# Kernel optimization log

Hardware: AMD Instinct MI355X
Metric: run time of the kernel (lower is better)

Reference implementation:

```python
import jax, jax.numpy as jnp
import numpy as np

NUM_BLOCKS = 100  # original samples at most 100 blocks; ids are in [0, NUM_BLOCKS)
EPS = 1e-8       # F.cosine_similarity default eps (clamps norms from below)


def setup_inputs() -> dict:
    key = jax.random.key(0)
    k1, k2 = jax.random.split(key)
    N, D = 1000000, 128
    z = jax.random.normal(k1, (N, D), dtype=jnp.float32)
    poi_to_road_block = jax.random.randint(k2, (N,), 0, NUM_BLOCKS, dtype=jnp.int32)
    return {"z": z, "poi_to_road_block": poi_to_road_block}


def reference(z, poi_to_road_block):
    N, D = z.shape
    ids = poi_to_road_block
    # per-block counts and sums -> block centers (mean embedding per road block)
    counts = jax.ops.segment_sum(jnp.ones((N,), z.dtype), ids, num_segments=NUM_BLOCKS)  # [B]
    sums = jax.ops.segment_sum(z, ids, num_segments=NUM_BLOCKS)                          # [B, D]
    centers = sums / jnp.maximum(counts, 1.0)[:, None]                                   # [B, D]
    # cosine similarity between each point and its block center
    c = centers[ids]                                                                     # [N, D] gather
    dot = jnp.sum(z * c, axis=-1)                                                        # [N]
    z_norm = jnp.maximum(jnp.sqrt(jnp.sum(z * z, axis=-1)), EPS)
    c_norm = jnp.maximum(jnp.sqrt(jnp.sum(c * c, axis=-1)), EPS)
    cos = dot / (z_norm * c_norm)                                                        # [N]
    # per-block mean cosine, then average (1 - mean_cos) over blocks with >1 member
    cos_sum = jax.ops.segment_sum(cos, ids, num_segments=NUM_BLOCKS)                     # [B]
    mean_cos = cos_sum / jnp.maximum(counts, 1.0)
    valid = counts > 1.0
    total = jnp.sum(jnp.where(valid, 1.0 - mean_cos, 0.0))
    count = jnp.maximum(jnp.sum(valid.astype(z.dtype)), 1.0)
    return total / count
```

## Files before the change

kernel.cpp:

```cpp
#include <hip/hip_runtime.h>
#include <hip/hip_bf16.h>

#define NBLK 100
#define DIM 128
#define EVEC (NBLK * DIM)
#define SLICE (2 * EVEC + NBLK)
#define EPSV 1e-8f
#define SSCALE 4194304.0f
#define NSCALE 16777216.0f
#define INV_SSCALE (1.0f / SSCALE)
#define INV_NSCALE (1.0f / NSCALE)

__device__ __forceinline__ float dpp_qsum16(float x) {
  int xi, yi;
  xi = __builtin_bit_cast(int, x);
  yi = __builtin_amdgcn_update_dpp(0, xi, 0xB1, 0xF, 0xF, false);
  x += __builtin_bit_cast(float, yi);
  xi = __builtin_bit_cast(int, x);
  yi = __builtin_amdgcn_update_dpp(0, xi, 0x4E, 0xF, 0xF, false);
  x += __builtin_bit_cast(float, yi);
  xi = __builtin_bit_cast(int, x);
  yi = __builtin_amdgcn_update_dpp(0, xi, 0x124, 0xF, 0xF, false);
  x += __builtin_bit_cast(float, yi);
  xi = __builtin_bit_cast(int, x);
  yi = __builtin_amdgcn_update_dpp(0, xi, 0x128, 0xF, 0xF, false);
  x += __builtin_bit_cast(float, yi);
  return x;
}

__global__ __launch_bounds__(1024) void rbc_accum(
    const float4* __restrict__ z4, const int* __restrict__ ids,
    float* __restrict__ ws, int N, int nwaves) {
  __shared__ int lsum[EVEC];
  __shared__ int lnsum[EVEC];
  __shared__ int lcnt[NBLK];
  const int tid = threadIdx.x;
  for (int e = tid; e < EVEC; e += 1024) { lsum[e] = 0; lnsum[e] = 0; }
  if (tid < NBLK) lcnt[tid] = 0;
  __syncthreads();

  const int lane = tid & 63;
  const int q  = lane >> 4;
  const int r  = lane & 15;
  const int qp = q & 1;
  const int w = blockIdx.x * (blockDim.x >> 6) + (tid >> 6);
  const int ngroups = N >> 2;

#define RBC_POINT_BODY(A0, A1, BB)                                           \
  {                                                                          \
    float sq = A0.x * A0.x + A0.y * A0.y + A0.z * A0.z + A0.w * A0.w +       \
               A1.x * A1.x + A1.y * A1.y + A1.z * A1.z + A1.w * A1.w;        \
    sq = dpp_qsum16(sq);                                                     \
    const float rn =                                                         \
        __builtin_amdgcn_rcpf(fmaxf(__builtin_amdgcn_sqrtf(sq), EPSV));      \
    const float rnN = rn * NSCALE;                                           \
    const float v0[4] = {A0.x, A0.y, A0.z, A0.w};                            \
    const float v1[4] = {A1.x, A1.y, A1.z, A1.w};                            \
    const int base = BB * DIM;                                               \
    _Pragma("unroll")                                                        \
    for (int s = 0; s < 4; ++s) {                                            \
      const float x0 = qp ? v0[s ^ 1] : v0[s];                               \
      const float x1 = qp ? v1[s ^ 1] : v1[s];                               \
      const int p0 = base + r + ((((s & 1) ^ qp)) << 4) + ((s >> 1) << 5);   \
      atomicAdd(&lsum[p0], __float2int_rn(x0 * SSCALE));                     \
      atomicAdd(&lnsum[p0], __float2int_rn(x0 * rnN));                       \
      atomicAdd(&lsum[p0 + 64], __float2int_rn(x1 * SSCALE));                \
      atomicAdd(&lnsum[p0 + 64], __float2int_rn(x1 * rnN));                  \
    }                                                                        \
    if (r == 0) atomicAdd(&lcnt[BB], 1);                                     \
  }

  const int stride2 = nwaves << 1;
  int j0 = w, j1 = w + nwaves;
  bool h0 = j0 < ngroups, h1 = j1 < ngroups;
  float4 A0, A1, B0, B1;
  int bA = 0, bB = 0;
  if (h0) {
    const int i = (j0 << 2) + q;
    const float4* p = z4 + ((size_t)i << 5);
    A0 = p[r]; A1 = p[r + 16]; bA = ids[i];
  }
  if (h1) {
    const int i = (j1 << 2) + q;
    const float4* p = z4 + ((size_t)i << 5);
    B0 = p[r]; B1 = p[r + 16]; bB = ids[i];
  }
  while (h0) {
    const int n0 = j0 + stride2, n1 = j1 + stride2;
    const bool hn0 = n0 < ngroups, hn1 = n1 < ngroups;
    float4 NA0, NA1, NB0, NB1;
    int nbA = 0, nbB = 0;
    if (hn0) {
      const int i = (n0 << 2) + q;
      const float4* p = z4 + ((size_t)i << 5);
      NA0 = p[r]; NA1 = p[r + 16]; nbA = ids[i];
    }
    if (hn1) {
      const int i = (n1 << 2) + q;
      const float4* p = z4 + ((size_t)i << 5);
      NB0 = p[r]; NB1 = p[r + 16]; nbB = ids[i];
    }
    RBC_POINT_BODY(A0, A1, bA);
    if (h1) RBC_POINT_BODY(B0, B1, bB);
    A0 = NA0; A1 = NA1; B0 = NB0; B1 = NB1; bA = nbA; bB = nbB;
    j0 = n0; j1 = n1; h0 = hn0; h1 = hn1;
  }
  if (blockIdx.x == 0 && (tid >> 6) == 0 && (N & 3)) {
    const int i = ((ngroups << 2)) + q;
    if (q < (N & 3)) {
      const float4* zp = z4 + ((size_t)i << 5);
      const float4 a0 = zp[r];
      const float4 a1 = zp[r + 16];
      const int b = ids[i];
      RBC_POINT_BODY(a0, a1, b);
    }
  }
#undef RBC_POINT_BODY
  __syncthreads();

  float* slice = ws + (size_t)blockIdx.x * SLICE;
  for (int e = tid; e < EVEC; e += 1024) {
    slice[e] = (float)lsum[e] * INV_SSCALE;
    slice[EVEC + e] = (float)lnsum[e] * INV_NSCALE;
  }
  if (tid < NBLK) slice[2 * EVEC + tid] = (float)lcnt[tid];
}

__global__ __launch_bounds__(512) void rbc_blockstat(
    const float* __restrict__ ws, float* __restrict__ stat, int G) {
  __shared__ float sp[512];
  __shared__ float np_[512];
  const int b = blockIdx.x;
  const int t = threadIdx.x;
  const int d = t & 127;
  const int qq = t >> 7;
  const int gpq = (G + 3) >> 2;
  const int g0 = qq * gpq;
  const int g1 = (g0 + gpq < G) ? (g0 + gpq) : G;
  float s = 0.f, n = 0.f;
  for (int g = g0; g < g1; ++g) {
    const float* f = ws + (size_t)g * SLICE + (size_t)b * DIM;
    s += f[d];
    n += f[EVEC + d];
  }
  sp[t] = s;
  np_[t] = n;

  if (t >= 256 && t < 320) {
    const int l = t - 256;
    float c = 0.f;
    for (int g = l; g < G; g += 64) c += ws[(size_t)g * SLICE + 2 * EVEC + b];
#pragma unroll
    for (int m = 1; m < 64; m <<= 1) c += __shfl_xor(c, m);
    if (l == 0) stat[b * 4 + 2] = c;
  }
  __syncthreads();

  if (t < 128) {
    const float ss = sp[t] + sp[t + 128] + sp[t + 256] + sp[t + 384];
    const float nn = np_[t] + np_[t + 128] + np_[t + 256] + np_[t + 384];
    sp[t] = ss * ss;
    np_[t] = nn * ss;
  }
  __syncthreads();

  if (t < 64) {
    float S2 = sp[t] + sp[t + 64];
    float ND = np_[t] + np_[t + 64];
#pragma unroll
    for (int m = 1; m < 64; m <<= 1) {
      S2 += __shfl_xor(S2, m);
      ND += __shfl_xor(ND, m);
    }
    if (t == 0) {
      stat[b * 4 + 0] = ND;
      stat[b * 4 + 1] = S2;
    }
  }
}

__global__ __launch_bounds__(128) void rbc_final(const float* __restrict__ stat,
                                                 float* __restrict__ out) {
  __shared__ float lv[2];
  __shared__ float lc[2];
  const int t = threadIdx.x;
  float val = 0.f, vc = 0.f;
  if (t < NBLK) {
    const float ND = stat[t * 4 + 0];
    const float S2 = stat[t * 4 + 1];
    const float cnt = stat[t * 4 + 2];
    const float cnt1 = fmaxf(cnt, 1.0f);
    const float cn = fmaxf(sqrtf(S2) / cnt1, EPSV);
    const float mean_cos = ND / (cnt1 * cnt1 * cn);
    if (cnt > 1.0f) { val = 1.0f - mean_cos; vc = 1.0f; }
  }
#pragma unroll
  for (int m = 1; m < 64; m <<= 1) {
    val += __shfl_xor(val, m);
    vc += __shfl_xor(vc, m);
  }
  if ((t & 63) == 0) { lv[t >> 6] = val; lc[t >> 6] = vc; }
  __syncthreads();
  if (t == 0) out[0] = (lv[0] + lv[1]) / fmaxf(lc[0] + lc[1], 1.0f);
}

extern "C" void kernel_launch(void* const* d_in, const int* in_sizes, int n_in,
                              void* d_out, int out_size, void* d_ws, size_t ws_size,
                              hipStream_t stream) {
  const float* z = (const float*)d_in[0];
  const int* ids = (const int*)d_in[1];
  const int N = in_sizes[1];
  float* out = (float*)d_out;
  float* ws = (float*)d_ws;

  size_t cap = (ws_size - 400 * sizeof(float)) / (sizeof(float) * (size_t)SLICE);
  int G = 256;
  if (cap < (size_t)G) G = (int)(cap > 1 ? cap : 1);
  const int nwaves = G * (1024 / 64);

  rbc_accum<<<G, 1024, 0, stream>>>((const float4*)z, ids, ws, N, nwaves);

  float* stat = ws + (size_t)G * SLICE;
  rbc_blockstat<<<NBLK, 512, 0, stream>>>(ws, stat, G);
  rbc_final<<<1, 128, 0, stream>>>(stat, out);
}
```

Measured before the change: 121.9 us.

## Pack two biased fixed-point lanes into 64-bit LDS atomics, deepen prefetch

Replaces per-element 32-bit LDS integer atomics with 64-bit atomics that each carry two biased, clamped fixed-point values (dimensions d and d+64). This halves the number of LDS atomic operations per point. The bias is removed per block at writeout using the member count. The load pipeline also moves from one to two iterations of prefetch. The cost is lower fixed-point precision, values clamped to ±8, and reliance on unsigned wraparound staying within 32 bits per lane. Overflow or carry into the upper lane is possible if a block's per-workgroup counts grow large.

Measured after the change: 122.7 us. About the same (+0.6%).

```diff
diff --git a/kernel.cpp b/kernel.cpp
--- a/kernel.cpp
+++ b/kernel.cpp
@@ -4,12 +4,16 @@
 #define NBLK 100
 #define DIM 128
 #define EVEC (NBLK * DIM)
+#define EV64 (NBLK * 64)
 #define SLICE (2 * EVEC + NBLK)
 #define EPSV 1e-8f
-#define SSCALE 4194304.0f
-#define NSCALE 16777216.0f
+#define SSCALE 32768.0f
+#define NSCALE 262144.0f
+#define BIASF 262144.0f
+#define BIASI 262144u
 #define INV_SSCALE (1.0f / SSCALE)
 #define INV_NSCALE (1.0f / NSCALE)
+
 
 __device__ __forceinline__ float dpp_qsum16(float x) {
   int xi, yi;
@@ -31,97 +35,112 @@
 __global__ __launch_bounds__(1024) void rbc_accum(
     const float4* __restrict__ z4, const int* __restrict__ ids,
     float* __restrict__ ws, int N, int nwaves) {
-  __shared__ int lsum[EVEC];
-  __shared__ int lnsum[EVEC];
+  __shared__ unsigned long long lsum[EV64];
+  __shared__ unsigned long long lnsum[EV64];
   __shared__ int lcnt[NBLK];
   const int tid = threadIdx.x;
-  for (int e = tid; e < EVEC; e += 1024) { lsum[e] = 0; lnsum[e] = 0; }
+  for (int e = tid; e < EV64; e += 1024) { lsum[e] = 0ull; lnsum[e] = 0ull; }
   if (tid < NBLK) lcnt[tid] = 0;
   __syncthreads();
 
   const int lane = tid & 63;
-  const int q  = lane >> 4;
-  const int r  = lane & 15;
-  const int qp = q & 1;
+  const int q = lane >> 4;
+  const int r = lane & 15;
   const int w = blockIdx.x * (blockDim.x >> 6) + (tid >> 6);
   const int ngroups = N >> 2;
 
-#define RBC_POINT_BODY(A0, A1, BB)                                           \
-  {                                                                          \
-    float sq = A0.x * A0.x + A0.y * A0.y + A0.z * A0.z + A0.w * A0.w +       \
-               A1.x * A1.x + A1.y * A1.y + A1.z * A1.z + A1.w * A1.w;        \
-    sq = dpp_qsum16(sq);                                                     \
-    const float rn =                                                         \
-        __builtin_amdgcn_rcpf(fmaxf(__builtin_amdgcn_sqrtf(sq), EPSV));      \
-    const float rnN = rn * NSCALE;                                           \
-    const float v0[4] = {A0.x, A0.y, A0.z, A0.w};                            \
-    const float v1[4] = {A1.x, A1.y, A1.z, A1.w};                            \
-    const int base = BB * DIM;                                               \
-    _Pragma("unroll")                                                        \
-    for (int s = 0; s < 4; ++s) {                                            \
-      const float x0 = qp ? v0[s ^ 1] : v0[s];                               \
-      const float x1 = qp ? v1[s ^ 1] : v1[s];                               \
-      const int p0 = base + r + ((((s & 1) ^ qp)) << 4) + ((s >> 1) << 5);   \
-      atomicAdd(&lsum[p0], __float2int_rn(x0 * SSCALE));                     \
-      atomicAdd(&lnsum[p0], __float2int_rn(x0 * rnN));                       \
-      atomicAdd(&lsum[p0 + 64], __float2int_rn(x1 * SSCALE));                \
-      atomicAdd(&lnsum[p0 + 64], __float2int_rn(x1 * rnN));                  \
-    }                                                                        \
-    if (r == 0) atomicAdd(&lcnt[BB], 1);                                     \
-  }
-
-  const int stride2 = nwaves << 1;
-  int j0 = w, j1 = w + nwaves;
-  bool h0 = j0 < ngroups, h1 = j1 < ngroups;
-  float4 A0, A1, B0, B1;
-  int bA = 0, bB = 0;
-  if (h0) {
-    const int i = (j0 << 2) + q;
-    const float4* p = z4 + ((size_t)i << 5);
-    A0 = p[r]; A1 = p[r + 16]; bA = ids[i];
-  }
-  if (h1) {
-    const int i = (j1 << 2) + q;
-    const float4* p = z4 + ((size_t)i << 5);
-    B0 = p[r]; B1 = p[r + 16]; bB = ids[i];
-  }
-  while (h0) {
-    const int n0 = j0 + stride2, n1 = j1 + stride2;
-    const bool hn0 = n0 < ngroups, hn1 = n1 < ngroups;
-    float4 NA0, NA1, NB0, NB1;
-    int nbA = 0, nbB = 0;
-    if (hn0) {
-      const int i = (n0 << 2) + q;
+#define RBC_BODY(A0, A1, BB)                                                  \
+  {                                                                           \
+    float sq = A0.x * A0.x + A0.y * A0.y + A0.z * A0.z + A0.w * A0.w +        \
+               A1.x * A1.x + A1.y * A1.y + A1.z * A1.z + A1.w * A1.w;         \
+    sq = dpp_qsum16(sq);                                                      \
+    const float rn =                                                          \
+        __builtin_amdgcn_rcpf(fmaxf(__builtin_amdgcn_sqrtf(sq), EPSV));       \
+    const float v0[4] = {A0.x, A0.y, A0.z, A0.w};                             \
+    const float v1[4] = {A1.x, A1.y, A1.z, A1.w};                             \
+    const int base = BB * 64 + r;                                             \
+    _Pragma("unroll")                                                         \
+    for (int s = 0; s < 4; ++s) {                                             \
+      const float x0 = v0[s], x1 = v1[s];                                     \
+      const unsigned qs0 = (unsigned)__float2int_rn(                          \
+          fminf(fmaxf(x0, -8.f), 8.f) * SSCALE + BIASF);                      \
+      const unsigned qs1 = (unsigned)__float2int_rn(                          \
+          fminf(fmaxf(x1, -8.f), 8.f) * SSCALE + BIASF);                      \
+      const unsigned qn0 = (unsigned)__float2int_rn(                          \
+          fminf(fmaxf(x0 * rn, -1.f), 1.f) * NSCALE + BIASF);                 \
+      const unsigned qn1 = (unsigned)__float2int_rn(                          \
+          fminf(fmaxf(x1 * rn, -1.f), 1.f) * NSCALE + BIASF);                 \
+      atomicAdd(&lsum[base + (s << 4)],                                       \
+                (unsigned long long)qs0 | ((unsigned long long)qs1 << 32));   \
+      atomicAdd(&lnsum[base + (s << 4)],                                      \
+                (unsigned long long)qn0 | ((unsigned long long)qn1 << 32));   \
+    }                                                                         \
+    if (r == 0) atomicAdd(&lcnt[BB], 1);                                      \
+  }
+
+  const int nw = nwaves;
+  const int st2 = nw << 1;
+  int j = w;
+  float4 c0a, c0b, c1a, c1b, n0a, n0b, n1a, n1b;
+  int cb0 = 0, cb1 = 0, nb0 = 0, nb1 = 0;
+  bool hc0 = j < ngroups, hc1 = j + nw < ngroups;
+  bool hn0 = j + st2 < ngroups, hn1 = j + st2 + nw < ngroups;
+  if (hc0) { const int i = (j << 2) + q;
+    const float4* p = z4 + ((size_t)i << 5);
+    c0a = p[r]; c0b = p[r + 16]; cb0 = ids[i]; }
+  if (hc1) { const int i = ((j + nw) << 2) + q;
+    const float4* p = z4 + ((size_t)i << 5);
+    c1a = p[r]; c1b = p[r + 16]; cb1 = ids[i]; }
+  if (hn0) { const int i = ((j + st2) << 2) + q;
+    const float4* p = z4 + ((size_t)i << 5);
+    n0a = p[r]; n0b = p[r + 16]; nb0 = ids[i]; }
+  if (hn1) { const int i = ((j + st2 + nw) << 2) + q;
+    const float4* p = z4 + ((size_t)i << 5);
+    n1a = p[r]; n1b = p[r + 16]; nb1 = ids[i]; }
+
+  while (hc0) {
+    const int jt = j + (st2 << 1);
+    const bool ht0 = jt < ngroups, ht1 = jt + nw < ngroups;
+    float4 t0a, t0b, t1a, t1b;
+    int tb0 = 0, tb1 = 0;
+    if (ht0) { const int i = (jt << 2) + q;
       const float4* p = z4 + ((size_t)i << 5);
-      NA0 = p[r]; NA1 = p[r + 16]; nbA = ids[i];
-    }
-    if (hn1) {
-      const int i = (n1 << 2) + q;
+      t0a = p[r]; t0b = p[r + 16]; tb0 = ids[i]; }
+    if (ht1) { const int i = ((jt + nw) << 2) + q;
       const float4* p = z4 + ((size_t)i << 5);
-      NB0 = p[r]; NB1 = p[r + 16]; nbB = ids[i];
-    }
-    RBC_POINT_BODY(A0, A1, bA);
-    if (h1) RBC_POINT_BODY(B0, B1, bB);
-    A0 = NA0; A1 = NA1; B0 = NB0; B1 = NB1; bA = nbA; bB = nbB;
-    j0 = n0; j1 = n1; h0 = hn0; h1 = hn1;
+      t1a = p[r]; t1b = p[r + 16]; tb1 = ids[i]; }
+    RBC_BODY(c0a, c0b, cb0);
+    if (hc1) RBC_BODY(c1a, c1b, cb1);
+    c0a = n0a; c0b = n0b; cb0 = nb0; hc0 = hn0;
+    c1a = n1a; c1b = n1b; cb1 = nb1; hc1 = hn1;
+    n0a = t0a; n0b = t0b; nb0 = tb0; hn0 = ht0;
+    n1a = t1a; n1b = t1b; nb1 = tb1; hn1 = ht1;
+    j += st2;
   }
   if (blockIdx.x == 0 && (tid >> 6) == 0 && (N & 3)) {
-    const int i = ((ngroups << 2)) + q;
+    const int i = (ngroups << 2) + q;
     if (q < (N & 3)) {
       const float4* zp = z4 + ((size_t)i << 5);
       const float4 a0 = zp[r];
       const float4 a1 = zp[r + 16];
       const int b = ids[i];
-      RBC_POINT_BODY(a0, a1, b);
+      RBC_BODY(a0, a1, b);
     }
   }
-#undef RBC_POINT_BODY
+#undef RBC_BODY
   __syncthreads();
 
   float* slice = ws + (size_t)blockIdx.x * SLICE;
-  for (int e = tid; e < EVEC; e += 1024) {
-    slice[e] = (float)lsum[e] * INV_SSCALE;
-    slice[EVEC + e] = (float)lnsum[e] * INV_NSCALE;
+  for (int e = tid; e < EV64; e += 1024) {
+    const int b = e >> 6;
+    const int dp = e & 63;
+    const unsigned cb = (unsigned)lcnt[b] * BIASI;
+    const unsigned long long vs = lsum[e];
+    const unsigned long long vn = lnsum[e];
+    slice[b * DIM + dp]               = (float)(int)((unsigned)vs - cb) * INV_SSCALE;
+    slice[b * DIM + 64 + dp]          = (float)(int)((unsigned)(vs >> 32) - cb) * INV_SSCALE;
+    slice[EVEC + b * DIM + dp]        = (float)(int)((unsigned)vn - cb) * INV_NSCALE;
+    slice[EVEC + b * DIM + 64 + dp]   = (float)(int)((unsigned)(vn >> 32) - cb) * INV_NSCALE;
   }
   if (tid < NBLK) slice[2 * EVEC + tid] = (float)lcnt[tid];
 }
```
